# Kernel tuning notes

Hardware: AMD Instinct MI355X
Metric: run time of the kernel (lower is better)

The kernel has to match this reference:

```python
import jax, jax.numpy as jnp
import numpy as np
from jax.scipy.linalg import cho_solve

N = 4096        # num nodes
D = 256         # in_dim == out_dim
NUM_HOPS = 2
R = 32          # subspace_dim
ETA = 0.5
EPS_SUB = 0.5   # eps in coeff = r / (n * eps^2)
LN_EPS = 1e-5


def setup_inputs() -> dict:
    rng = np.random.default_rng(0)
    K = NUM_HOPS + 1
    # sparse-ish binary adjacency mask with self loops
    mask = (rng.random((N, N)) < 0.002).astype(np.float32)
    mask = np.maximum(mask, np.eye(N, dtype=np.float32))
    deg = mask.sum(axis=1, keepdims=True)
    A = (mask / deg).astype(np.float32)          # row-stochastic propagation
    L = (np.eye(N, dtype=np.float32) - A)        # normalized Laplacian
    H = rng.standard_normal((N, D)).astype(np.float32)
    # orthonormal subspace bases per hop, as in __init__ (QR of randn)
    U = np.stack([np.linalg.qr(rng.standard_normal((D, R)))[0][:, :R] for _ in range(K)]).astype(np.float32)
    lambda_laps = np.full((K,), 0.1, dtype=np.float32)
    hop_weights = np.full((K,), 1.0 / K, dtype=np.float32)
    threshold = np.full((D,), 0.05, dtype=np.float32)
    gamma = np.ones((D,), dtype=np.float32)
    beta = np.zeros((D,), dtype=np.float32)
    return {
        "H": jnp.asarray(H), "A": jnp.asarray(A), "adj_mask": jnp.asarray(mask),
        "L": jnp.asarray(L), "U": jnp.asarray(U),
        "lambda_laps": jnp.asarray(lambda_laps), "hop_weights": jnp.asarray(hop_weights),
        "threshold": jnp.asarray(threshold), "gamma": jnp.asarray(gamma), "beta": jnp.asarray(beta),
    }


def reference(H, A, adj_mask, L, U, lambda_laps, hop_weights, threshold, gamma, beta):
    n, d = H.shape
    r = U.shape[-1]
    # multi-hop propagation
    hops = [H]
    Hk = H
    for _ in range(NUM_HOPS):
        Hk = A @ Hk
        hops.append(Hk)
    w = jax.nn.softmax(hop_weights)
    laps = jax.nn.softplus(lambda_laps)
    coeff = r / (n * EPS_SUB ** 2)
    neg = (1.0 - adj_mask) * -1e9
    I_r = jnp.eye(r, dtype=H.dtype)
    agg = jnp.zeros_like(H)        # accumulates grad_k.T, shape [n, d]
    lap_total = jnp.zeros_like(H)
    for k, H_k in enumerate(hops):
        Uk = U[k]                  # [d, r]
        Zk = Uk.T @ H_k.T          # [r, n]
        M = I_r + coeff * (Zk @ Zk.T)              # [r, r], SPD
        Lc = jnp.linalg.cholesky(M)
        M_inv = cho_solve((Lc, True), I_r)         # cholesky_inverse
        MZ = M_inv @ Zk                            # [r, n]
        scores = Zk.T @ MZ + neg                   # [n, n] masked subspace attention
        alpha = jax.nn.softmax(scores, axis=1)
        grad_k = (Uk @ (MZ @ alpha.T)).T           # [n, d]
        agg = agg + w[k] * grad_k
        lap_total = lap_total + laps[k] * (L @ H_k)
    H_half = H + ETA * agg - ETA * lap_total
    # soft-threshold (proj is None since in_dim == out_dim)
    H_out = jnp.sign(H_half) * jax.nn.relu(jnp.abs(H_half) - threshold[None, :])
    H_out = H_out + H              # residual
    mu = H_out.mean(axis=-1, keepdims=True)
    var = H_out.var(axis=-1, keepdims=True)
    H_out = (H_out - mu) / jnp.sqrt(var + LN_EPS) * gamma + beta
    # orthogonality loss over all (k, l) pairs
    K = U.shape[0]
    orth_loss = jnp.asarray(0.0, dtype=H.dtype)
    for k in range(K):
        for l in range(k, K):
            G = U[k].T @ U[l]
            orth_loss = orth_loss + jnp.sum(((G - I_r) if l == k else G) ** 2)
    lap_smooth = jnp.sum(H_out * (L @ H_out))  # trace(H^T L H)
    return H_out, orth_loss, lap_smooth, jax.lax.stop_gradient(w)
```

## Files before the change

### kernel.cpp

```cpp
#include <hip/hip_runtime.h>
#include <math.h>

#define NN 4096
#define DD 256
#define KK 3
#define RR 32
#define MAXNNZ 128

static constexpr float ETA    = 0.5f;
static constexpr float COEFF  = 0.03125f;
static constexpr float LN_EPSF = 1e-5f;

#define OFF_H1   0
#define OFF_H2   (NN*DD)
#define OFF_H3   (2*NN*DD)
#define OFF_Y    (3*NN*DD)
#define OFF_W    (OFF_Y + KK*NN*RR)
#define OFF_P    (OFF_W + KK*NN*RR)
#define OFF_M    (OFF_P + KK*NN*RR)
#define OFF_MINV (OFF_M + KK*RR*RR)
#define OFF_SCAL (OFF_MINV + KK*RR*RR)
#define OFF_NNZ  (OFF_SCAL + 8)
#define OFF_COLS (OFF_NNZ + NN)
#define OFF_VALS (OFF_COLS + NN*MAXNNZ)
#define OFF_PART (OFF_VALS + NN*MAXNNZ)
#define OFF_ORTH (OFF_PART + NN/4)

__global__ __launch_bounds__(1024) void k_prep_orth(const float* __restrict__ hw,
                       const float* __restrict__ ll, const float* __restrict__ U,
                       float* __restrict__ ws, float* __restrict__ out) {
  int b = blockIdx.x;
  int t = threadIdx.x;
  if (b == 6) {
    if (t == 0) {
      float m = fmaxf(fmaxf(hw[0], hw[1]), hw[2]);
      float e0 = expf(hw[0]-m), e1 = expf(hw[1]-m), e2 = expf(hw[2]-m);
      float s = e0 + e1 + e2;
      float w0 = e0/s, w1 = e1/s, w2 = e2/s;
      ws[OFF_SCAL+0] = w0; ws[OFF_SCAL+1] = w1; ws[OFF_SCAL+2] = w2;
      for (int k = 0; k < KK; ++k) {
        float x = ll[k];
        ws[OFF_SCAL+3+k] = (x > 20.f) ? x : log1pf(expf(x));
      }
      out[NN*DD + 2] = w0; out[NN*DD + 3] = w1; out[NN*DD + 4] = w2;
    }
    for (int idx = t; idx < KK*RR*RR; idx += 1024) {
      int rr2 = idx % (RR*RR);
      ws[OFF_M + idx] = ((rr2 / RR) == (rr2 % RR)) ? 1.f : 0.f;
    }
    return;
  }
  int p = b;
  int k = (p < 3) ? 0 : ((p < 5) ? 1 : 2);
  int l = (p < 3) ? p : ((p < 5) ? p - 2 : 2);
  int a = t >> 5, bb = t & 31;
  float s = 0.f;
  for (int dd = 0; dd < DD; ++dd)
    s += U[(size_t)k*DD*RR + dd*RR + a] * U[(size_t)l*DD*RR + dd*RR + bb];
  if (k == l && a == bb) s -= 1.f;
  float sq = s * s;
  __shared__ float red[1024];
  red[t] = sq;
  __syncthreads();
  for (int st = 512; st > 0; st >>= 1) {
    if (t < st) red[t] += red[t + st];
    __syncthreads();
  }
  if (t == 0) ws[OFF_ORTH + p] = red[0];
}

__global__ void k_csr(const float* __restrict__ A, int* __restrict__ nnz,
                      int* __restrict__ cols, float* __restrict__ vals) {
  int i = blockIdx.x;
  __shared__ int cnt;
  if (threadIdx.x == 0) cnt = 0;
  __syncthreads();
  const float4* row4 = (const float4*)(A + (size_t)i * NN);
  for (int j0 = 0; j0 < NN/4; j0 += 256) {
    float4 v = row4[j0 + threadIdx.x];
    int jb = (j0 + threadIdx.x) * 4;
    if (v.x != 0.f) { int p = atomicAdd(&cnt,1); if (p<MAXNNZ){cols[i*MAXNNZ+p]=jb+0; vals[i*MAXNNZ+p]=v.x;} }
    if (v.y != 0.f) { int p = atomicAdd(&cnt,1); if (p<MAXNNZ){cols[i*MAXNNZ+p]=jb+1; vals[i*MAXNNZ+p]=v.y;} }
    if (v.z != 0.f) { int p = atomicAdd(&cnt,1); if (p<MAXNNZ){cols[i*MAXNNZ+p]=jb+2; vals[i*MAXNNZ+p]=v.z;} }
    if (v.w != 0.f) { int p = atomicAdd(&cnt,1); if (p<MAXNNZ){cols[i*MAXNNZ+p]=jb+3; vals[i*MAXNNZ+p]=v.w;} }
  }
  __syncthreads();
  int n = cnt < MAXNNZ ? cnt : MAXNNZ;
  int npad = (n + 7) & ~7;
  for (int e = n + threadIdx.x; e < npad; e += 256) {
    cols[i*MAXNNZ + e] = i;
    vals[i*MAXNNZ + e] = 0.f;
  }
  if (threadIdx.x == 0) nnz[i] = n;
}

__global__ void k_spmvy(const float* __restrict__ X, float* __restrict__ Hout,
                        const int* __restrict__ nnz, const int* __restrict__ cols,
                        const float* __restrict__ vals,
                        const float* __restrict__ Uo, float* __restrict__ Yo,
                        const float* __restrict__ Un, float* __restrict__ Yn) {
  int t = threadIdx.x;
  int r = t >> 6, lane = t & 63;
  int row = blockIdx.x * 4 + r;
  int d4 = lane * 4;
  int n = nnz[row];
  int npad = (n + 7) & ~7;
  const int* ci = cols + row*MAXNNZ;
  const float* vi = vals + row*MAXNNZ;
  float4 acc = {0.f, 0.f, 0.f, 0.f};
  float4 own = {0.f, 0.f, 0.f, 0.f};
  for (int e0 = 0; e0 < npad; e0 += 8) {
    int4 c0 = *(const int4*)(ci + e0);
    int4 c1 = *(const int4*)(ci + e0 + 4);
    float4 v0 = *(const float4*)(vi + e0);
    float4 v1 = *(const float4*)(vi + e0 + 4);
    float4 x0 = *(const float4*)(X + (size_t)c0.x*DD + d4);
    float4 x1 = *(const float4*)(X + (size_t)c0.y*DD + d4);
    float4 x2 = *(const float4*)(X + (size_t)c0.z*DD + d4);
    float4 x3 = *(const float4*)(X + (size_t)c0.w*DD + d4);
    float4 x4 = *(const float4*)(X + (size_t)c1.x*DD + d4);
    float4 x5 = *(const float4*)(X + (size_t)c1.y*DD + d4);
    float4 x6 = *(const float4*)(X + (size_t)c1.z*DD + d4);
    float4 x7 = *(const float4*)(X + (size_t)c1.w*DD + d4);
    if (c0.x == row) own = x0;
    if (c0.y == row) own = x1;
    if (c0.z == row) own = x2;
    if (c0.w == row) own = x3;
    if (c1.x == row) own = x4;
    if (c1.y == row) own = x5;
    if (c1.z == row) own = x6;
    if (c1.w == row) own = x7;
    acc.x += v0.x*x0.x + v0.y*x1.x + v0.z*x2.x + v0.w*x3.x + v1.x*x4.x + v1.y*x5.x + v1.z*x6.x + v1.w*x7.x;
    acc.y += v0.x*x0.y + v0.y*x1.y + v0.z*x2.y + v0.w*x3.y + v1.x*x4.y + v1.y*x5.y + v1.z*x6.y + v1.w*x7.y;
    acc.z += v0.x*x0.z + v0.y*x1.z + v0.z*x2.z + v0.w*x3.z + v1.x*x4.z + v1.y*x5.z + v1.z*x6.z + v1.w*x7.z;
    acc.w += v0.x*x0.w + v0.y*x1.w + v0.z*x2.w + v0.w*x3.w + v1.x*x4.w + v1.y*x5.w + v1.z*x6.w + v1.w*x7.w;
  }
  *(float4*)(Hout + (size_t)row*DD + d4) = acc;
  if (!Uo && !Un) return;
  __shared__ float Hs[4][2][DD];
  *(float4*)&Hs[r][0][d4] = own;
  *(float4*)&Hs[r][1][d4] = acc;
  __syncthreads();
  int c = lane & 31, h = lane >> 5;
  if (Uo) {
    float part = 0.f;
    #pragma unroll 8
    for (int d = h*128; d < h*128 + 128; ++d) part += Hs[r][0][d] * Uo[d*RR + c];
    part += __shfl_xor(part, 32, 64);
    if (h == 0) Yo[(size_t)row*RR + c] = part;
  }
  if (Un) {
    float part = 0.f;
    #pragma unroll 8
    for (int d = h*128; d < h*128 + 128; ++d) part += Hs[r][1][d] * Un[d*RR + c];
    part += __shfl_xor(part, 32, 64);
    if (h == 0) Yn[(size_t)row*RR + c] = part;
  }
}

__global__ __launch_bounds__(1024) void k_gram(const float* __restrict__ Y, float* __restrict__ M) {
  int k = blockIdx.y;
  __shared__ float Ys[128*RR];
  int t = threadIdx.x;
  const float* Yk = Y + (size_t)k*NN*RR + (size_t)blockIdx.x*128*RR;
  for (int idx = t; idx < 128*RR; idx += 1024) Ys[idx] = Yk[idx];
  __syncthreads();
  int a = t >> 5, b = t & 31;
  float s = 0.f;
  for (int i = 0; i < 128; ++i) s += Ys[i*RR + a] * Ys[i*RR + b];
  atomicAdd(&M[k*RR*RR + a*RR + b], COEFF * s);
}

__global__ __launch_bounds__(256) void k_gj(const float* __restrict__ M, float* __restrict__ Minv) {
  int k = blockIdx.x;
  __shared__ float B[RR][2*RR];
  int t = threadIdx.x;
  for (int idx = t; idx < RR*2*RR; idx += 256) {
    int r = idx >> 6, c = idx & 63;
    B[r][c] = (c < RR) ? M[k*RR*RR + r*RR + c] : ((c - RR == r) ? 1.f : 0.f);
  }
  __syncthreads();
  int c = t & 63, r0 = t >> 6;
  for (int j = 0; j < RR; ++j) {
    float bjc = B[j][c];
    float pinv = 1.f / B[j][j];
    float f[8];
    #pragma unroll
    for (int q = 0; q < 8; ++q) f[q] = B[r0 + 4*q][j];
    __syncthreads();
    float pb = pinv * bjc;
    #pragma unroll
    for (int q = 0; q < 8; ++q) {
      int r = r0 + 4*q;
      B[r][c] = (r == j) ? pb : (B[r][c] - f[q] * pb);
    }
    __syncthreads();
  }
  for (int idx = t; idx < RR*RR; idx += 256) {
    int r = idx >> 5, cc = idx & 31;
    Minv[k*RR*RR + r*RR + cc] = B[r][RR + cc];
  }
}

__global__ void k_wproj(const float* __restrict__ Y, const float* __restrict__ Minv,
                        float* __restrict__ W) {
  int k = blockIdx.y;
  __shared__ float Ms[RR*RR];
  __shared__ float Ys[8*RR];
  int t = threadIdx.x;
  for (int idx = t; idx < RR*RR; idx += 256) Ms[idx] = Minv[k*RR*RR + idx];
  int row0 = blockIdx.x * 8;
  Ys[t] = Y[(size_t)k*NN*RR + (size_t)row0*RR + t];
  __syncthreads();
  int rl = t >> 5, c = t & 31;
  float acc = 0.f;
  for (int a = 0; a < RR; ++a) acc += Ys[rl*RR + a] * Ms[a*RR + c];
  W[(size_t)k*NN*RR + (size_t)(row0+rl)*RR + c] = acc;
}

__global__ void k_attn(const float* __restrict__ Y, const float* __restrict__ W,
                       float* __restrict__ P, const int* __restrict__ nnz,
                       const int* __restrict__ cols) {
  int i = blockIdx.x, k = blockIdx.y;
  int t = threadIdx.x;
  const float* Yk = Y + (size_t)k*NN*RR;
  const float* Wk = W + (size_t)k*NN*RR;
  int n = nnz[i];
  int npad = (n + 7) & ~7;
  const int* ci = cols + i*MAXNNZ;
  __shared__ float Ys[RR];
  __shared__ float sc[MAXNNZ];
  if (t < RR) Ys[t] = Yk[(size_t)i*RR + t];
  sc[t] = -1e30f; sc[t+64] = -1e30f;
  __syncthreads();
  for (int e = t; e < npad; e += 64) {
    const float4* wr = (const float4*)(Wk + (size_t)ci[e]*RR);
    float s = 0.f;
    #pragma unroll
    for (int q = 0; q < 8; ++q) {
      float4 wv = wr[q];
      s += wv.x*Ys[4*q] + wv.y*Ys[4*q+1] + wv.z*Ys[4*q+2] + wv.w*Ys[4*q+3];
    }
    sc[e] = (e < n) ? s : -1e30f;
  }
  __syncthreads();
  float s0 = sc[t], s1 = sc[t+64];
  float m = fmaxf(s0, s1);
  #pragma unroll
  for (int o = 32; o > 0; o >>= 1) m = fmaxf(m, __shfl_xor(m, o, 64));
  float e0v = expf(s0 - m), e1v = expf(s1 - m);
  sc[t] = e0v; sc[t+64] = e1v;
  float l = e0v + e1v;
  #pragma unroll
  for (int o = 32; o > 0; o >>= 1) l += __shfl_xor(l, o, 64);
  float linv = 1.f / l;
  __syncthreads();
  int c = t & 31, h = t >> 5;
  float acc = 0.f;
  for (int e = h; e < npad; e += 2) acc += sc[e] * Wk[(size_t)ci[e]*RR + c];
  acc += __shfl_xor(acc, 32, 64);
  if (t < RR) P[(size_t)k*NN*RR + (size_t)i*RR + t] = acc * linv;
}

__global__ void k_epi(const float* __restrict__ H0, const float* __restrict__ ws,
                      const float* __restrict__ U, const float* __restrict__ thr,
                      const float* __restrict__ gma, const float* __restrict__ bta,
                      float* __restrict__ out) {
  __shared__ float Us[DD][RR+1];
  __shared__ float Ps[8][KK*RR];
  int t = threadIdx.x;
  int ty = t >> 5, tx = t & 31;
  int row0 = blockIdx.x * 8;
  const float* P    = ws + OFF_P;
  const float* scal = ws + OFF_SCAL;
  for (int idx = t; idx < 8*KK*RR; idx += 256) {
    int rl = idx / (KK*RR), kr = idx % (KK*RR);
    int k = kr / RR, rr2 = kr % RR;
    Ps[rl][kr] = P[(size_t)k*NN*RR + (size_t)(row0+rl)*RR + rr2];
  }
  float lp0 = scal[3], lp1 = scal[4], lp2 = scal[5];
  float gacc[8];
  #pragma unroll
  for (int j = 0; j < 8; ++j) gacc[j] = 0.f;
  for (int k = 0; k < KK; ++k) {
    __syncthreads();
    for (int idx = t; idx < DD*RR; idx += 256) Us[idx >> 5][idx & 31] = U[(size_t)k*DD*RR + idx];
    __syncthreads();
    float wk = scal[k];
    #pragma unroll
    for (int j = 0; j < 8; ++j) {
      int d = tx + 32*j;
      float s = 0.f;
      #pragma unroll
      for (int rr2 = 0; rr2 < RR; ++rr2) s += Ps[ty][k*RR + rr2] * Us[d][rr2];
      gacc[j] += wk * s;
    }
  }
  int i = row0 + ty;
  const float* H1 = ws + OFF_H1;
  const float* H2 = ws + OFF_H2;
  const float* H3 = ws + OFF_H3;
  float v[8]; float sum = 0.f, sumsq = 0.f;
  #pragma unroll
  for (int j = 0; j < 8; ++j) {
    int d = tx + 32*j;
    size_t idx = (size_t)i*DD + d;
    float h0 = H0[idx], h1 = H1[idx], h2 = H2[idx], h3 = H3[idx];
    float lap = lp0*(h0-h1) + lp1*(h1-h2) + lp2*(h2-h3);
    float hf = h0 + ETA*gacc[j] - ETA*lap;
    float a = fabsf(hf) - thr[d];
    float sft = (a > 0.f) ? copysignf(a, hf) : 0.f;
    float x = sft + h0;
    v[j] = x; sum += x; sumsq += x*x;
  }
  #pragma unroll
  for (int o = 16; o > 0; o >>= 1) {
    sum   += __shfl_xor(sum, o, 32);
    sumsq += __shfl_xor(sumsq, o, 32);
  }
  float mu  = sum * (1.f/DD);
  float var = sumsq * (1.f/DD) - mu*mu;
  float inv = rsqrtf(var + LN_EPSF);
  #pragma unroll
  for (int j = 0; j < 8; ++j) {
    int d = tx + 32*j;
    out[(size_t)i*DD + d] = (v[j] - mu) * inv * gma[d] + bta[d];
  }
}

__global__ void k_lapsm(const float* __restrict__ Hout, const int* __restrict__ nnz,
                        const int* __restrict__ cols, const float* __restrict__ vals,
                        float* __restrict__ partial) {
  int t = threadIdx.x;
  int row = blockIdx.x * 4 + (t >> 6);
  int d4 = (t & 63) * 4;
  int n = nnz[row];
  int npad = (n + 7) & ~7;
  const int* ci = cols + row*MAXNNZ;
  const float* vi = vals + row*MAXNNZ;
  float4 acc = {0.f, 0.f, 0.f, 0.f};
  for (int e0 = 0; e0 < npad; e0 += 8) {
    int4 c0 = *(const int4*)(ci + e0);
    int4 c1 = *(const int4*)(ci + e0 + 4);
    float4 v0 = *(const float4*)(vi + e0);
    float4 v1 = *(const float4*)(vi + e0 + 4);
    float4 x0 = *(const float4*)(Hout + (size_t)c0.x*DD + d4);
    float4 x1 = *(const float4*)(Hout + (size_t)c0.y*DD + d4);
    float4 x2 = *(const float4*)(Hout + (size_t)c0.z*DD + d4);
    float4 x3 = *(const float4*)(Hout + (size_t)c0.w*DD + d4);
    float4 x4 = *(const float4*)(Hout + (size_t)c1.x*DD + d4);
    float4 x5 = *(const float4*)(Hout + (size_t)c1.y*DD + d4);
    float4 x6 = *(const float4*)(Hout + (size_t)c1.z*DD + d4);
    float4 x7 = *(const float4*)(Hout + (size_t)c1.w*DD + d4);
    acc.x += v0.x*x0.x + v0.y*x1.x + v0.z*x2.x + v0.w*x3.x + v1.x*x4.x + v1.y*x5.x + v1.z*x6.x + v1.w*x7.x;
    acc.y += v0.x*x0.y + v0.y*x1.y + v0.z*x2.y + v0.w*x3.y + v1.x*x4.y + v1.y*x5.y + v1.z*x6.y + v1.w*x7.y;
    acc.z += v0.x*x0.z + v0.y*x1.z + v0.z*x2.z + v0.w*x3.z + v1.x*x4.z + v1.y*x5.z + v1.z*x6.z + v1.w*x7.z;
    acc.w += v0.x*x0.w + v0.y*x1.w + v0.z*x2.w + v0.w*x3.w + v1.x*x4.w + v1.y*x5.w + v1.z*x6.w + v1.w*x7.w;
  }
  float4 h = *(const float4*)(Hout + (size_t)row*DD + d4);
  float part = h.x*(h.x-acc.x) + h.y*(h.y-acc.y) + h.z*(h.z-acc.z) + h.w*(h.w-acc.w);
  #pragma unroll
  for (int o = 32; o > 0; o >>= 1) part += __shfl_xor(part, o, 64);
  __shared__ float red[4];
  if ((t & 63) == 0) red[t >> 6] = part;
  __syncthreads();
  if (t == 0) partial[blockIdx.x] = red[0] + red[1] + red[2] + red[3];
}

__global__ void k_red(const float* __restrict__ ws, float* __restrict__ out) {
  const float* partial = ws + OFF_PART;
  int t = threadIdx.x;
  float4 p = *(const float4*)(partial + t*4);
  float s = p.x + p.y + p.z + p.w;
  #pragma unroll
  for (int o = 32; o > 0; o >>= 1) s += __shfl_xor(s, o, 64);
  __shared__ float red[4];
  if ((t & 63) == 0) red[t >> 6] = s;
  __syncthreads();
  if (t == 0) {
    out[1] = red[0] + red[1] + red[2] + red[3];
    const float* op = ws + OFF_ORTH;
    out[0] = op[0] + op[1] + op[2] + op[3] + op[4] + op[5];
  }
}

extern "C" void kernel_launch(void* const* d_in, const int* in_sizes, int n_in,
                              void* d_out, int out_size, void* d_ws, size_t ws_size,
                              hipStream_t stream) {
  const float* H   = (const float*)d_in[0];
  const float* A   = (const float*)d_in[1];
  const float* U   = (const float*)d_in[4];
  const float* ll  = (const float*)d_in[5];
  const float* hw  = (const float*)d_in[6];
  const float* thr = (const float*)d_in[7];
  const float* gma = (const float*)d_in[8];
  const float* bta = (const float*)d_in[9];
  float* out = (float*)d_out;
  float* ws  = (float*)d_ws;
  int* nnz   = (int*)(ws + OFF_NNZ);
  int* cols  = (int*)(ws + OFF_COLS);
  float* vals = ws + OFF_VALS;
  float* Y = ws + OFF_Y;

  k_prep_orth<<<7, 1024, 0, stream>>>(hw, ll, U, ws, out);
  k_csr<<<NN, 256, 0, stream>>>(A, nnz, cols, vals);
  k_spmvy<<<NN/4, 256, 0, stream>>>(H, ws + OFF_H1, nnz, cols, vals,
                                    U, Y, U + (size_t)DD*RR, Y + (size_t)NN*RR);
  k_spmvy<<<NN/4, 256, 0, stream>>>(ws + OFF_H1, ws + OFF_H2, nnz, cols, vals,
                                    nullptr, nullptr, U + (size_t)2*DD*RR, Y + (size_t)2*NN*RR);
  k_spmvy<<<NN/4, 256, 0, stream>>>(ws + OFF_H2, ws + OFF_H3, nnz, cols, vals,
                                    nullptr, nullptr, nullptr, nullptr);
  dim3 g32(NN/128, KK);
  k_gram<<<g32, 1024, 0, stream>>>(Y, ws + OFF_M);
  k_gj<<<KK, 256, 0, stream>>>(ws + OFF_M, ws + OFF_MINV);
  dim3 g512(NN/8, KK);
  k_wproj<<<g512, 256, 0, stream>>>(Y, ws + OFF_MINV, ws + OFF_W);
  dim3 gattn(NN, KK);
  k_attn<<<gattn, 64, 0, stream>>>(Y, ws + OFF_W, ws + OFF_P, nnz, cols);
  k_epi<<<NN/8, 256, 0, stream>>>(H, ws, U, thr, gma, bta, out);
  k_lapsm<<<NN/4, 256, 0, stream>>>(out, nnz, cols, vals, ws + OFF_PART);
  k_red<<<1, 256, 0, stream>>>(ws, out + NN*DD);
}
```

Measured before the change: 300.7 us.

## Fuse kernels, merge gram and inverse via last-block, drop W projection buffer

Cuts the launch count from 12 to 7. The CSR build is merged with the prep/orth work, and the third SpMV is merged with the gram accumulation; the last-arriving block, found through an atomic counter, then runs Gauss-Jordan inversion for all three hops. The materialised W = Y·Minv projection is removed: attention folds Minv into a per-row query vector, then applies Minv to the aggregated value vector, which also shrinks workspace traffic. The final reduction is fused into the Laplacian-smoothness kernel through another last-block counter, at the cost of serialising the three small inversions inside one block.

After: 410.9 us. +36.7%, slower.

```diff
diff --git a/kernel.cpp b/kernel.cpp
--- a/kernel.cpp
+++ b/kernel.cpp
@@ -15,8 +15,7 @@
 #define OFF_H2   (NN*DD)
 #define OFF_H3   (2*NN*DD)
 #define OFF_Y    (3*NN*DD)
-#define OFF_W    (OFF_Y + KK*NN*RR)
-#define OFF_P    (OFF_W + KK*NN*RR)
+#define OFF_P    (OFF_Y + KK*NN*RR)
 #define OFF_M    (OFF_P + KK*NN*RR)
 #define OFF_MINV (OFF_M + KK*RR*RR)
 #define OFF_SCAL (OFF_MINV + KK*RR*RR)
@@ -25,60 +24,71 @@
 #define OFF_VALS (OFF_COLS + NN*MAXNNZ)
 #define OFF_PART (OFF_VALS + NN*MAXNNZ)
 #define OFF_ORTH (OFF_PART + NN/4)
-
-__global__ __launch_bounds__(1024) void k_prep_orth(const float* __restrict__ hw,
-                       const float* __restrict__ ll, const float* __restrict__ U,
-                       float* __restrict__ ws, float* __restrict__ out) {
+#define OFF_CTR  (OFF_ORTH + 8)
+
+__global__ void k_csr_prep(const float* __restrict__ A, int* __restrict__ nnz,
+                           int* __restrict__ cols, float* __restrict__ vals,
+                           const float* __restrict__ hw, const float* __restrict__ ll,
+                           const float* __restrict__ U,
+                           float* __restrict__ ws, float* __restrict__ out) {
   int b = blockIdx.x;
   int t = threadIdx.x;
-  if (b == 6) {
-    if (t == 0) {
-      float m = fmaxf(fmaxf(hw[0], hw[1]), hw[2]);
-      float e0 = expf(hw[0]-m), e1 = expf(hw[1]-m), e2 = expf(hw[2]-m);
-      float s = e0 + e1 + e2;
-      float w0 = e0/s, w1 = e1/s, w2 = e2/s;
-      ws[OFF_SCAL+0] = w0; ws[OFF_SCAL+1] = w1; ws[OFF_SCAL+2] = w2;
-      for (int k = 0; k < KK; ++k) {
-        float x = ll[k];
-        ws[OFF_SCAL+3+k] = (x > 20.f) ? x : log1pf(expf(x));
+  if (b >= NN) {
+    int p = b - NN;
+    if (p == 6) {
+      if (t == 0) {
+        float m = fmaxf(fmaxf(hw[0], hw[1]), hw[2]);
+        float e0 = expf(hw[0]-m), e1 = expf(hw[1]-m), e2 = expf(hw[2]-m);
+        float s = e0 + e1 + e2;
+        float w0 = e0/s, w1 = e1/s, w2 = e2/s;
+        ws[OFF_SCAL+0] = w0; ws[OFF_SCAL+1] = w1; ws[OFF_SCAL+2] = w2;
+        for (int k = 0; k < KK; ++k) {
+          float x = ll[k];
+          ws[OFF_SCAL+3+k] = (x > 20.f) ? x : log1pf(expf(x));
+        }
+        out[NN*DD + 2] = w0; out[NN*DD + 3] = w1; out[NN*DD + 4] = w2;
+        ((int*)(ws + OFF_CTR))[0] = 0;
+        ((int*)(ws + OFF_CTR))[1] = 0;
       }
-      out[NN*DD + 2] = w0; out[NN*DD + 3] = w1; out[NN*DD + 4] = w2;
-    }
-    for (int idx = t; idx < KK*RR*RR; idx += 1024) {
-      int rr2 = idx % (RR*RR);
-      ws[OFF_M + idx] = ((rr2 / RR) == (rr2 % RR)) ? 1.f : 0.f;
-    }
+      for (int idx = t; idx < KK*RR*RR; idx += 256) {
+        int rr2 = idx % (RR*RR);
+        ws[OFF_M + idx] = ((rr2 / RR) == (rr2 % RR)) ? 1.f : 0.f;
+      }
+      return;
+    }
+    int k = (p < 3) ? 0 : ((p < 5) ? 1 : 2);
+    int l = (p < 3) ? p : ((p < 5) ? p - 2 : 2);
+    int a0 = t >> 5, bb = t & 31;
+    float s0 = 0.f, s1 = 0.f, s2 = 0.f, s3 = 0.f;
+    for (int dd = 0; dd < DD; ++dd) {
+      float ul = U[(size_t)l*DD*RR + dd*RR + bb];
+      const float* uk = U + (size_t)k*DD*RR + dd*RR;
+      s0 += uk[a0]      * ul;
+      s1 += uk[a0 + 8]  * ul;
+      s2 += uk[a0 + 16] * ul;
+      s3 += uk[a0 + 24] * ul;
+    }
+    if (k == l && bb == a0)      s0 -= 1.f;
+    if (k == l && bb == a0 + 8)  s1 -= 1.f;
+    if (k == l && bb == a0 + 16) s2 -= 1.f;
+    if (k == l && bb == a0 + 24) s3 -= 1.f;
+    float sq = s0*s0 + s1*s1 + s2*s2 + s3*s3;
+    #pragma unroll
+    for (int o = 32; o > 0; o >>= 1) sq += __shfl_xor(sq, o, 64);
+    __shared__ float red[4];
+    if ((t & 63) == 0) red[t >> 6] = sq;
+    __syncthreads();
+    if (t == 0) ws[OFF_ORTH + p] = red[0] + red[1] + red[2] + red[3];
     return;
   }
-  int p = b;
-  int k = (p < 3) ? 0 : ((p < 5) ? 1 : 2);
-  int l = (p < 3) ? p : ((p < 5) ? p - 2 : 2);
-  int a = t >> 5, bb = t & 31;
-  float s = 0.f;
-  for (int dd = 0; dd < DD; ++dd)
-    s += U[(size_t)k*DD*RR + dd*RR + a] * U[(size_t)l*DD*RR + dd*RR + bb];
-  if (k == l && a == bb) s -= 1.f;
-  float sq = s * s;
-  __shared__ float red[1024];
-  red[t] = sq;
-  __syncthreads();
-  for (int st = 512; st > 0; st >>= 1) {
-    if (t < st) red[t] += red[t + st];
-    __syncthreads();
-  }
-  if (t == 0) ws[OFF_ORTH + p] = red[0];
-}
-
-__global__ void k_csr(const float* __restrict__ A, int* __restrict__ nnz,
-                      int* __restrict__ cols, float* __restrict__ vals) {
-  int i = blockIdx.x;
+  int i = b;
   __shared__ int cnt;
-  if (threadIdx.x == 0) cnt = 0;
+  if (t == 0) cnt = 0;
   __syncthreads();
   const float4* row4 = (const float4*)(A + (size_t)i * NN);
   for (int j0 = 0; j0 < NN/4; j0 += 256) {
-    float4 v = row4[j0 + threadIdx.x];
-    int jb = (j0 + threadIdx.x) * 4;
+    float4 v = row4[j0 + t];
+    int jb = (j0 + t) * 4;
     if (v.x != 0.f) { int p = atomicAdd(&cnt,1); if (p<MAXNNZ){cols[i*MAXNNZ+p]=jb+0; vals[i*MAXNNZ+p]=v.x;} }
     if (v.y != 0.f) { int p = atomicAdd(&cnt,1); if (p<MAXNNZ){cols[i*MAXNNZ+p]=jb+1; vals[i*MAXNNZ+p]=v.y;} }
     if (v.z != 0.f) { int p = atomicAdd(&cnt,1); if (p<MAXNNZ){cols[i*MAXNNZ+p]=jb+2; vals[i*MAXNNZ+p]=v.z;} }
@@ -87,11 +97,11 @@
   __syncthreads();
   int n = cnt < MAXNNZ ? cnt : MAXNNZ;
   int npad = (n + 7) & ~7;
-  for (int e = n + threadIdx.x; e < npad; e += 256) {
+  for (int e = n + t; e < npad; e += 256) {
     cols[i*MAXNNZ + e] = i;
     vals[i*MAXNNZ + e] = 0.f;
   }
-  if (threadIdx.x == 0) nnz[i] = n;
+  if (t == 0) nnz[i] = n;
 }
 
 __global__ void k_spmvy(const float* __restrict__ X, float* __restrict__ Hout,
@@ -158,88 +168,128 @@
   }
 }
 
-__global__ __launch_bounds__(1024) void k_gram(const float* __restrict__ Y, float* __restrict__ M) {
-  int k = blockIdx.y;
+__global__ __launch_bounds__(256) void k_spmv_gram(const float* __restrict__ X,
+                        float* __restrict__ Hout,
+                        const int* __restrict__ nnz, const int* __restrict__ cols,
+                        const float* __restrict__ vals,
+                        const float* __restrict__ Y, float* __restrict__ M,
+                        float* __restrict__ Minv, int* __restrict__ ctr) {
+  int t = threadIdx.x;
+  if (blockIdx.x < NN/4) {
+    int r = t >> 6, lane = t & 63;
+    int row = blockIdx.x * 4 + r;
+    int d4 = lane * 4;
+    int n = nnz[row];
+    int npad = (n + 7) & ~7;
+    const int* ci = cols + row*MAXNNZ;
+    const float* vi = vals + row*MAXNNZ;
+    float4 acc = {0.f, 0.f, 0.f, 0.f};
+    for (int e0 = 0; e0 < npad; e0 += 8) {
+      int4 c0 = *(const int4*)(ci + e0);
+      int4 c1 = *(const int4*)(ci + e0 + 4);
+      float4 v0 = *(const float4*)(vi + e0);
+      float4 v1 = *(const float4*)(vi + e0 + 4);
+      float4 x0 = *(const float4*)(X + (size_t)c0.x*DD + d4);
+      float4 x1 = *(const float4*)(X + (size_t)c0.y*DD + d4);
+      float4 x2 = *(const float4*)(X + (size_t)c0.z*DD + d4);
+      float4 x3 = *(const float4*)(X + (size_t)c0.w*DD + d4);
+      float4 x4 = *(const float4*)(X + (size_t)c1.x*DD + d4);
+      float4 x5 = *(const float4*)(X + (size_t)c1.y*DD + d4);
+      float4 x6 = *(const float4*)(X + (size_t)c1.z*DD + d4);
+      float4 x7 = *(const float4*)(X + (size_t)c1.w*DD + d4);
+      acc.x += v0.x*x0.x + v0.y*x1.x + v0.z*x2.x + v0.w*x3.x + v1.x*x4.x + v1.y*x5.x + v1.z*x6.x + v1.w*x7.x;
+      acc.y += v0.x*x0.y + v0.y*x1.y + v0.z*x2.y + v0.w*x3.y + v1.x*x4.y + v1.y*x5.y + v1.z*x6.y + v1.w*x7.y;
+      acc.z += v0.x*x0.z + v0.y*x1.z + v0.z*x2.z + v0.w*x3.z + v1.x*x4.z + v1.y*x5.z + v1.z*x6.z + v1.w*x7.z;
+      acc.w += v0.x*x0.w + v0.y*x1.w + v0.z*x2.w + v0.w*x3.w + v1.x*x4.w + v1.y*x5.w + v1.z*x6.w + v1.w*x7.w;
+    }
+    *(float4*)(Hout + (size_t)row*DD + d4) = acc;
+    return;
+  }
+  int g = blockIdx.x - NN/4;
+  int k = g >> 5, chunk = g & 31;
   __shared__ float Ys[128*RR];
-  int t = threadIdx.x;
-  const float* Yk = Y + (size_t)k*NN*RR + (size_t)blockIdx.x*128*RR;
-  for (int idx = t; idx < 128*RR; idx += 1024) Ys[idx] = Yk[idx];
-  __syncthreads();
-  int a = t >> 5, b = t & 31;
-  float s = 0.f;
-  for (int i = 0; i < 128; ++i) s += Ys[i*RR + a] * Ys[i*RR + b];
-  atomicAdd(&M[k*RR*RR + a*RR + b], COEFF * s);
-}
-
-__global__ __launch_bounds__(256) void k_gj(const float* __restrict__ M, float* __restrict__ Minv) {
-  int k = blockIdx.x;
+  const float* Yk = Y + (size_t)k*NN*RR + (size_t)chunk*128*RR;
+  for (int idx = t; idx < 128*RR; idx += 256) Ys[idx] = Yk[idx];
+  __syncthreads();
+  #pragma unroll
+  for (int q = 0; q < 4; ++q) {
+    int cell = t + q*256;
+    int a = cell >> 5, bb = cell & 31;
+    float s = 0.f;
+    for (int i = 0; i < 128; ++i) s += Ys[i*RR + a] * Ys[i*RR + bb];
+    atomicAdd(&M[k*RR*RR + a*RR + bb], COEFF * s);
+  }
+  __threadfence();
+  __shared__ int amLast;
+  if (t == 0) amLast = (atomicAdd(ctr, 1) == 95) ? 1 : 0;
+  __syncthreads();
+  if (!amLast) return;
+  __threadfence();
   __shared__ float B[RR][2*RR];
-  int t = threadIdx.x;
-  for (int idx = t; idx < RR*2*RR; idx += 256) {
-    int r = idx >> 6, c = idx & 63;
-    B[r][c] = (c < RR) ? M[k*RR*RR + r*RR + c] : ((c - RR == r) ? 1.f : 0.f);
-  }
-  __syncthreads();
-  int c = t & 63, r0 = t >> 6;
-  for (int j = 0; j < RR; ++j) {
-    float bjc = B[j][c];
-    float pinv = 1.f / B[j][j];
-    float f[8];
-    #pragma unroll
-    for (int q = 0; q < 8; ++q) f[q] = B[r0 + 4*q][j];
+  for (int kk2 = 0; kk2 < KK; ++kk2) {
+    for (int idx = t; idx < RR*2*RR; idx += 256) {
+      int r = idx >> 6, c = idx & 63;
+      float mv;
+      if (c < RR)
+        mv = __hip_atomic_load(&M[kk2*RR*RR + r*RR + c], __ATOMIC_RELAXED, __HIP_MEMORY_SCOPE_AGENT);
+      else
+        mv = (c - RR == r) ? 1.f : 0.f;
+      B[r][c] = mv;
+    }
     __syncthreads();
-    float pb = pinv * bjc;
-    #pragma unroll
-    for (int q = 0; q < 8; ++q) {
-      int r = r0 + 4*q;
-      B[r][c] = (r == j) ? pb : (B[r][c] - f[q] * pb);
-    }
+    int c = t & 63, r0 = t >> 6;
+    for (int j = 0; j < RR; ++j) {
+      float bjc = B[j][c];
+      float pinv = 1.f / B[j][j];
+      float f[8];
+      #pragma unroll
+      for (int q = 0; q < 8; ++q) f[q] = B[r0 + 4*q][j];
+      __syncthreads();
+      float pb = pinv * bjc;
+      #pragma unroll
+      for (int q = 0; q < 8; ++q) {
+        int r = r0 + 4*q;
+        B[r][c] = (r == j) ? pb : (B[r][c] - f[q] * pb);
+      }
+      __syncthreads();
+    }
+    for (int idx = t; idx < RR*RR; idx += 256)
+      Minv[kk2*RR*RR + (idx >> 5)*RR + (idx & 31)] = B[idx >> 5][RR + (idx & 31)];
     __syncthreads();
   }
-  for (int idx = t; idx < RR*RR; idx += 256) {
-    int r = idx >> 5, cc = idx & 31;
-    Minv[k*RR*RR + r*RR + cc] = B[r][RR + cc];
-  }
-}
-
-__global__ void k_wproj(const float* __restrict__ Y, const float* __restrict__ Minv,
-                        float* __restrict__ W) {
-  int k = blockIdx.y;
-  __shared__ float Ms[RR*RR];
-  __shared__ float Ys[8*RR];
-  int t = threadIdx.x;
-  for (int idx = t; idx < RR*RR; idx += 256) Ms[idx] = Minv[k*RR*RR + idx];
-  int row0 = blockIdx.x * 8;
-  Ys[t] = Y[(size_t)k*NN*RR + (size_t)row0*RR + t];
-  __syncthreads();
-  int rl = t >> 5, c = t & 31;
-  float acc = 0.f;
-  for (int a = 0; a < RR; ++a) acc += Ys[rl*RR + a] * Ms[a*RR + c];
-  W[(size_t)k*NN*RR + (size_t)(row0+rl)*RR + c] = acc;
-}
-
-__global__ void k_attn(const float* __restrict__ Y, const float* __restrict__ W,
+}
+
+__global__ void k_attn(const float* __restrict__ Y, const float* __restrict__ Minv,
                        float* __restrict__ P, const int* __restrict__ nnz,
                        const int* __restrict__ cols) {
   int i = blockIdx.x, k = blockIdx.y;
   int t = threadIdx.x;
   const float* Yk = Y + (size_t)k*NN*RR;
-  const float* Wk = W + (size_t)k*NN*RR;
-  int n = nnz[i];
-  int npad = (n + 7) & ~7;
+  __shared__ float Mi[RR*RR];
+  __shared__ float Yi[RR];
+  __shared__ float qv[RR];
+  __shared__ float sc[MAXNNZ];
+  __shared__ float vsum[RR];
+  for (int idx = t; idx < RR*RR; idx += 64) Mi[idx] = Minv[k*RR*RR + idx];
+  if (t < RR) Yi[t] = Yk[(size_t)i*RR + t];
+  sc[t] = -1e30f; sc[t+64] = -1e30f;
+  __syncthreads();
+  if (t < RR) {
+    float s = 0.f;
+    #pragma unroll 8
+    for (int a = 0; a < RR; ++a) s += Mi[a*RR + t] * Yi[a];
+    qv[t] = s;
+  }
+  __syncthreads();
+  int n = nnz[i], npad = (n + 7) & ~7;
   const int* ci = cols + i*MAXNNZ;
-  __shared__ float Ys[RR];
-  __shared__ float sc[MAXNNZ];
-  if (t < RR) Ys[t] = Yk[(size_t)i*RR + t];
-  sc[t] = -1e30f; sc[t+64] = -1e30f;
-  __syncthreads();
   for (int e = t; e < npad; e += 64) {
-    const float4* wr = (const float4*)(Wk + (size_t)ci[e]*RR);
+    const float4* yr = (const float4*)(Yk + (size_t)ci[e]*RR);
     float s = 0.f;
     #pragma unroll
-    for (int q = 0; q < 8; ++q) {
-      float4 wv = wr[q];
-      s += wv.x*Ys[4*q] + wv.y*Ys[4*q+1] + wv.z*Ys[4*q+2] + wv.w*Ys[4*q+3];
+    for (int qq = 0; qq < 8; ++qq) {
+      float4 yv = yr[qq];
+      s += yv.x*qv[4*qq] + yv.y*qv[4*qq+1] + yv.z*qv[4*qq+2] + yv.w*qv[4*qq+3];
     }
     sc[e] = (e < n) ? s : -1e30f;
   }
@@ -257,9 +307,16 @@
   __syncthreads();
   int c = t & 31, h = t >> 5;
   float acc = 0.f;
-  for (int e = h; e < npad; e += 2) acc += sc[e] * Wk[(size_t)ci[e]*RR + c];
+  for (int e = h; e < npad; e += 2) acc += sc[e] * Yk[(size_t)ci[e]*RR + c];
   acc += __shfl_xor(acc, 32, 64);
-  if (t < RR) P[(size_t)k*NN*RR + (size_t)i*RR + t] = acc * linv;
+  if (t < RR) vsum[t] = acc * linv;
+  __syncthreads();
+  if (t < RR) {
+    float s = 0.f;
+    #pragma unroll 8
+    for (int a = 0; a < RR; ++a) s += Mi[a*RR + t] * vsum[a];
+    P[(size_t)k*NN*RR + (size_t)i*RR + t] = s;
+  }
 }
 
 __global__ void k_epi(const float* __restrict__ H0, const float* __restrict__ ws,
@@ -328,9 +385,11 @@
   }
 }
 
-__global__ void k_lapsm(const float* __restrict__ Hout, const int* __restrict__ nnz,
-                        const int* __restrict__ cols, const float* __restrict__ vals,
-                        float* __restrict__ partial) {
+__global__ void k_lapsm_red(const float* __restrict__ Hout, const int* __restrict__ nnz,
+                            const int* __restrict__ cols, const float* __restrict__ vals,
+                            float* __restrict__ ws, int* __restrict__ ctr,
+                            float* __restrict__ out) {
+  float* partial = ws + OFF_PART;
   int t = threadIdx.x;
   int row = blockIdx.x * 4 + (t >> 6);
   int d4 = (t & 63) * 4;
@@ -357,30 +416,34 @@
     acc.z += v0.x*x0.z + v0.y*x1.z + v0.z*x2.z + v0.w*x3.z + v1.x*x4.z + v1.y*x5.z + v1.z*x6.z + v1.w*x7.z;
     acc.w += v0.x*x0.w + v0.y*x1.w + v0.z*x2.w + v0.w*x3.w + v1.x*x4.w + v1.y*x5.w + v1.z*x6.w + v1.w*x7.w;
   }
-  float4 h = *(const float4*)(Hout + (size_t)row*DD + d4);
-  float part = h.x*(h.x-acc.x) + h.y*(h.y-acc.y) + h.z*(h.z-acc.z) + h.w*(h.w-acc.w);
+  float4 hh = *(const float4*)(Hout + (size_t)row*DD + d4);
+  float part = hh.x*(hh.x-acc.x) + hh.y*(hh.y-acc.y) + hh.z*(hh.z-acc.z) + hh.w*(hh.w-acc.w);
   #pragma unroll
   for (int o = 32; o > 0; o >>= 1) part += __shfl_xor(part, o, 64);
   __shared__ float red[4];
   if ((t & 63) == 0) red[t >> 6] = part;
   __syncthreads();
   if (t == 0) partial[blockIdx.x] = red[0] + red[1] + red[2] + red[3];
-}
-
-__global__ void k_red(const float* __restrict__ ws, float* __restrict__ out) {
-  const float* partial = ws + OFF_PART;
-  int t = threadIdx.x;
-  float4 p = *(const float4*)(partial + t*4);
-  float s = p.x + p.y + p.z + p.w;
+  __threadfence();
+  __shared__ int amLast;
+  if (t == 0) amLast = (atomicAdd(ctr, 1) == (NN/4 - 1)) ? 1 : 0;
+  __syncthreads();
+  if (!amLast) return;
+  __threadfence();
+  float s = 0.f;
+  for (int idx = t; idx < NN/4; idx += 256)
+    s += __hip_atomic_load(&partial[idx], __ATOMIC_RELAXED, __HIP_MEMORY_SCOPE_AGENT);
   #pragma unroll
   for (int o = 32; o > 0; o >>= 1) s += __shfl_xor(s, o, 64);
-  __shared__ float red[4];
   if ((t & 63) == 0) red[t >> 6] = s;
   __syncthreads();
   if (t == 0) {
     out[1] = red[0] + red[1] + red[2] + red[3];
     const float* op = ws + OFF_ORTH;
-    out[0] = op[0] + op[1] + op[2] + op[3] + op[4] + op[5];
+    float orth = 0.f;
+    for (int p = 0; p < 6; ++p)
+      orth += __hip_atomic_load((float*)&op[p], __ATOMIC_RELAXED, __HIP_MEMORY_SCOPE_AGENT);
+    out[0] = orth;
   }
 }
 
@@ -400,24 +463,18 @@
   int* nnz   = (int*)(ws + OFF_NNZ);
   int* cols  = (int*)(ws + OFF_COLS);
   float* vals = ws + OFF_VALS;
+  int* ctr   = (int*)(ws + OFF_CTR);
   float* Y = ws + OFF_Y;
 
-  k_prep_orth<<<7, 1024, 0, stream>>>(hw, ll, U, ws, out);
-  k_csr<<<NN, 256, 0, stream>>>(A, nnz, cols, vals);
+  k_csr_prep<<<NN + 7, 256, 0, stream>>>(A, nnz, cols, vals, hw, ll, U, ws, out);
   k_spmvy<<<NN/4, 256, 0, stream>>>(H, ws + OFF_H1, nnz, cols, vals,
                                     U, Y, U + (size_t)DD*RR, Y + (size_t)NN*RR);
   k_spmvy<<<NN/4, 256, 0, stream>>>(ws + OFF_H1, ws + OFF_H2, nnz, cols, vals,
                                     nullptr, nullptr, U + (size_t)2*DD*RR, Y + (size_t)2*NN*RR);
-  k_spmvy<<<NN/4, 256, 0, stream>>>(ws + OFF_H2, ws + OFF_H3, nnz, cols, vals,
-                                    nullptr, nullptr, nullptr, nullptr);
-  dim3 g32(NN/128, KK);
-  k_gram<<<g32, 1024, 0, stream>>>(Y, ws + OFF_M);
-  k_gj<<<KK, 256, 0, stream>>>(ws + OFF_M, ws + OFF_MINV);
-  dim3 g512(NN/8, KK);
-  k_wproj<<<g512, 256, 0, stream>>>(Y, ws + OFF_MINV, ws + OFF_W);
+  k_spmv_gram<<<NN/4 + 96, 256, 0, stream>>>(ws + OFF_H2, ws + OFF_H3, nnz, cols, vals,
+                                             Y, ws + OFF_M, ws + OFF_MINV, ctr);
   dim3 gattn(NN, KK);
-  k_attn<<<gattn, 64, 0, stream>>>(Y, ws + OFF_W, ws + OFF_P, nnz, cols);
+  k_attn<<<gattn, 64, 0, stream>>>(Y, ws + OFF_MINV, ws + OFF_P, nnz, cols);
   k_epi<<<NN/8, 256, 0, stream>>>(H, ws, U, thr, gma, bta, out);
-  k_lapsm<<<NN/4, 256, 0, stream>>>(out, nnz, cols, vals, ws + OFF_PART);
-  k_red<<<1, 256, 0, stream>>>(ws, out + NN*DD);
-}
+  k_lapsm_red<<<NN/4, 256, 0, stream>>>(out, nnz, cols, vals, ws, ctr + 1, out + NN*DD);
+}
```
